# Kernel optimization log

Hardware: AMD Instinct MI355X
Metric: run time of the kernel (lower is better)

Reference implementation:

```python
import jax, jax.numpy as jnp
import numpy as np

NUM_HEADS = 16
KEY_DEPTH = 1024


def setup_inputs() -> dict:
    key = jax.random.key(0)
    ks = jax.random.split(key, 7)
    B, L, D = 2, 2048, 1024
    scale = 1.0 / np.sqrt(D)
    return {
        "query_antecedent": jax.random.normal(ks[0], (B, L, D), jnp.float32),
        "memory_antecedent": jax.random.normal(ks[1], (B, L, D), jnp.float32),
        "bias": jax.random.normal(ks[2], (1, 1, L, L), jnp.float32),
        "Wq": jax.random.normal(ks[3], (D, KEY_DEPTH), jnp.float32) * scale,
        "Wk": jax.random.normal(ks[4], (D, KEY_DEPTH), jnp.float32) * scale,
        "Wv": jax.random.normal(ks[5], (D, KEY_DEPTH), jnp.float32) * scale,
        "Wo": jax.random.normal(ks[6], (KEY_DEPTH, D), jnp.float32) * scale,
    }


def _split_heads(x, h):
    # [B, L, D] -> [B, H, L, D/H]
    b, l, d = x.shape
    return x.reshape(b, l, h, d // h).transpose(0, 2, 1, 3)


def reference(query_antecedent, memory_antecedent, bias, Wq, Wk, Wv, Wo):
    h = NUM_HEADS
    d_head = KEY_DEPTH // h
    q = _split_heads(query_antecedent @ Wq, h) * (d_head ** -0.5)
    k = _split_heads(memory_antecedent @ Wk, h)
    v = _split_heads(memory_antecedent @ Wv, h)
    # [B, H, Lq, Lk]
    logits = jnp.einsum("bhqd,bhkd->bhqk", q, k) + bias
    weights = jax.nn.softmax(logits, axis=-1)
    x = jnp.einsum("bhqk,bhkd->bhqd", weights, v)
    # combine heads: [B, H, L, d] -> [B, L, H*d]
    b, _, l, d = x.shape
    x = x.transpose(0, 2, 1, 3).reshape(b, l, h * d)
    return x @ Wo
```

## Files before the change

### kernel.cpp

```cpp
#include <hip/hip_runtime.h>
#include <hip/hip_bf16.h>


typedef __attribute__((ext_vector_type(8))) short short8;
typedef __attribute__((ext_vector_type(4))) short short4v;
typedef __attribute__((ext_vector_type(4))) float float4v;

#define BATCH 2
#define LSEQ 2048
#define DMODEL 1024
#define NHEADS 16
#define DHEAD 64
#define MROWS 4096
#define QKVLD 3072

__global__ __launch_bounds__(256)
void convert_kernel(const float* __restrict__ qa, const float* __restrict__ ma,
                    __hip_bfloat16* __restrict__ qo, __hip_bfloat16* __restrict__ mo)
{
    const size_t i = ((size_t)blockIdx.x * 256 + threadIdx.x) * 8;
    const float* src = blockIdx.y ? ma : qa;
    __hip_bfloat16* dst = blockIdx.y ? mo : qo;
    float4 v0 = *reinterpret_cast<const float4*>(src + i);
    float4 v1 = *reinterpret_cast<const float4*>(src + i + 4);
    union { __hip_bfloat16 h[8]; int4 v; } pk;
    pk.h[0] = (__hip_bfloat16)v0.x; pk.h[1] = (__hip_bfloat16)v0.y;
    pk.h[2] = (__hip_bfloat16)v0.z; pk.h[3] = (__hip_bfloat16)v0.w;
    pk.h[4] = (__hip_bfloat16)v1.x; pk.h[5] = (__hip_bfloat16)v1.y;
    pk.h[6] = (__hip_bfloat16)v1.z; pk.h[7] = (__hip_bfloat16)v1.w;
    *reinterpret_cast<int4*>(dst + i) = pk.v;
}

__global__ __launch_bounds__(256)
void transpose_w_kernel(const float* __restrict__ W0, const float* __restrict__ W1,
                        const float* __restrict__ W2, const float* __restrict__ W3,
                        __hip_bfloat16* __restrict__ T0, __hip_bfloat16* __restrict__ T1,
                        __hip_bfloat16* __restrict__ T2, __hip_bfloat16* __restrict__ T3)
{
    __shared__ __hip_bfloat16 T[64][68];

    const float* W; __hip_bfloat16* D;
    if      (blockIdx.z == 0) { W = W0; D = T0; }
    else if (blockIdx.z == 1) { W = W1; D = T1; }
    else if (blockIdx.z == 2) { W = W2; D = T2; }
    else                      { W = W3; D = T3; }

    const int t  = threadIdx.x;
    const int n0 = blockIdx.x * 64;
    const int k0 = blockIdx.y * 64;

#pragma unroll
    for (int p = 0; p < 4; ++p) {
        const int r = p * 16 + (t >> 4);
        const int c = (t & 15) * 4;
        float4 v = *reinterpret_cast<const float4*>(&W[(size_t)(k0 + r) * DMODEL + n0 + c]);
        union { __hip_bfloat16 h[4]; ushort4 v; } pk;
        pk.h[0] = (__hip_bfloat16)v.x; pk.h[1] = (__hip_bfloat16)v.y;
        pk.h[2] = (__hip_bfloat16)v.z; pk.h[3] = (__hip_bfloat16)v.w;
        *reinterpret_cast<ushort4*>(&T[r][c]) = pk.v;
    }
    __syncthreads();
#pragma unroll
    for (int p = 0; p < 2; ++p) {
        const int n  = p * 32 + (t & 31);
        const int kc = (t >> 5) * 8;
        union { __hip_bfloat16 h[8]; int4 v; } pk;
#pragma unroll
        for (int j = 0; j < 8; ++j) pk.h[j] = T[kc + j][n];
        *reinterpret_cast<int4*>(&D[(size_t)(n0 + n) * DMODEL + k0 + kc]) = pk.v;
    }
}

#define GBK 64

template<int BMT>
__global__ __launch_bounds__(256, 2)
void gemm_bt_kernel(const __hip_bfloat16* __restrict__ A0,
                    const __hip_bfloat16* __restrict__ A1, int nsplit,
                    float alpha0, float alpha1,
                    const __hip_bfloat16* __restrict__ Bt,
                    float* __restrict__ Cf, __hip_bfloat16* __restrict__ Cb,
                    int K, int ldc, int nbx)
{
    __shared__ __hip_bfloat16 As[BMT][GBK];
    __shared__ __hip_bfloat16 Bs[128][GBK];

    const int t    = threadIdx.x;
    const int w    = t >> 6;
    const int lane = t & 63;
    const int l15  = lane & 15;
    const int lq   = lane >> 4;
    const int wm   = (w >> 1) * (BMT / 2);
    const int wn   = (w & 1) * 64;
    const int MI   = BMT / 32;

    const int nwg  = gridDim.x;
    const int c    = blockIdx.x & 7;
    const int q    = blockIdx.x >> 3;
    const int mper = (nwg >> 3) / nbx;
    const int m0   = (c * mper + q / nbx) * BMT;
    const int n0   = (q % nbx) * 128;

    const __hip_bfloat16* A = (n0 < nsplit) ? A0 : A1;
    const float alpha = (n0 < nsplit) ? alpha0 : alpha1;

    const int lrow = lane >> 3;
    const int lch  = (lane & 7) ^ lrow;

    float4v acc[BMT / 32][4];
#pragma unroll
    for (int mi = 0; mi < MI; ++mi)
#pragma unroll
        for (int ni = 0; ni < 4; ++ni) acc[mi][ni] = (float4v){0.f, 0.f, 0.f, 0.f};

    for (int k0 = 0; k0 < K; k0 += GBK) {
        __syncthreads();
#pragma unroll
        for (int i = 0; i < BMT / 32; ++i) {
            const int rb = (w * (BMT / 32) + i) * 8;
            const int r  = rb + lrow;
            __builtin_amdgcn_global_load_lds(
                (const __attribute__((address_space(1))) void*)
                    (A + (size_t)(m0 + r) * K + k0 + lch * 8),
                (__attribute__((address_space(3))) void*)&As[rb][0], 16, 0, 0);
        }
#pragma unroll
        for (int i = 0; i < 4; ++i) {
            const int rb = (w * 4 + i) * 8;
            const int r  = rb + lrow;
            __builtin_amdgcn_global_load_lds(
                (const __attribute__((address_space(1))) void*)
                    (Bt + (size_t)(n0 + r) * K + k0 + lch * 8),
                (__attribute__((address_space(3))) void*)&Bs[rb][0], 16, 0, 0);
        }
        asm volatile("s_waitcnt vmcnt(0)" ::: "memory");
        __syncthreads();

#pragma unroll
        for (int kh = 0; kh < 2; ++kh) {
            short8 af[BMT / 32], bf[4];
#pragma unroll
            for (int mi = 0; mi < MI; ++mi) {
                const int r = wm + mi * 16 + l15;
                af[mi] = *reinterpret_cast<const short8*>(
                    &As[r][(((kh << 2) | lq) ^ (r & 7)) << 3]);
            }
#pragma unroll
            for (int ni = 0; ni < 4; ++ni) {
                const int r = wn + ni * 16 + l15;
                bf[ni] = *reinterpret_cast<const short8*>(
                    &Bs[r][(((kh << 2) | lq) ^ (r & 7)) << 3]);
            }
#pragma unroll
            for (int mi = 0; mi < MI; ++mi)
#pragma unroll
                for (int ni = 0; ni < 4; ++ni)
                    acc[mi][ni] = __builtin_amdgcn_mfma_f32_16x16x32_bf16(
                        af[mi], bf[ni], acc[mi][ni], 0, 0, 0);
        }
    }

#pragma unroll
    for (int mi = 0; mi < MI; ++mi)
#pragma unroll
        for (int ni = 0; ni < 4; ++ni)
#pragma unroll
            for (int r = 0; r < 4; ++r) {
                const int row = m0 + wm + mi * 16 + lq * 4 + r;
                const int col = n0 + wn + ni * 16 + l15;
                const float v = acc[mi][ni][r] * alpha;
                if (Cf) Cf[(size_t)row * ldc + col] = v;
                else    Cb[(size_t)row * ldc + col] = (__hip_bfloat16)v;
            }
}

#define KSTR 68
#define PSTR 132
#define NT (LSEQ / 128)

__global__ __launch_bounds__(512, 4)
void attn_mfma_kernel(const __hip_bfloat16* __restrict__ QKV,
                      const float* __restrict__ bias,
                      __hip_bfloat16* __restrict__ X)
{
    __shared__ __hip_bfloat16 Ks[2][128][KSTR];
    __shared__ __hip_bfloat16 Vt[2][64][PSTR];

    const int t   = threadIdx.x;
    const int w   = t >> 6;
    const int l15 = t & 15;
    const int lq  = (t & 63) >> 4;

    const int bid = blockIdx.x;
    const int r8  = bid & 7;
    const int j   = bid >> 3;
    const int bh  = r8 + 8 * (j >> 4);
    const int q0  = (j & 15) * 128;
    const int b   = bh >> 4;
    const int h   = bh & 15;

    const __hip_bfloat16* Kb = QKV + (size_t)b * LSEQ * QKVLD + 1024 + h * DHEAD;
    const __hip_bfloat16* Vb = Kb + 1024;

    short8 aq[2];
    {
        const __hip_bfloat16* qrow = QKV +
            (size_t)(b * LSEQ + q0 + w * 16 + l15) * QKVLD + h * DHEAD + lq * 8;
        aq[0] = *reinterpret_cast<const short8*>(qrow);
        aq[1] = *reinterpret_cast<const short8*>(qrow + 32);
    }

    const float* bp = bias + (size_t)(q0 + w * 16 + l15) * LSEQ + lq * 4;

    float lsum = 0.f;
    float4v o_acc[4];
#pragma unroll
    for (int n = 0; n < 4; ++n) o_acc[n] = (float4v){0.f, 0.f, 0.f, 0.f};

    const int skey = t >> 2;
    const int sdh  = (t & 3) * 16;
    const int a    = t & 3;
    const int cblk = ((skey >> 5) << 2) | ((skey >> 2) & 3);
    const int vcol = (((cblk ^ (a << 2)) << 3)) | ((((skey >> 4) & 1) << 2)) | (skey & 3);

    int4 pk0, pk1, pv0, pv1;
    {
        const __hip_bfloat16* ks = Kb + (size_t)skey * QKVLD + sdh;
        pk0 = *reinterpret_cast<const int4*>(ks);
        pk1 = *reinterpret_cast<const int4*>(ks + 8);
        const __hip_bfloat16* vs = Vb + (size_t)skey * QKVLD + sdh;
        pv0 = *reinterpret_cast<const int4*>(vs);
        pv1 = *reinterpret_cast<const int4*>(vs + 8);
    }
    *reinterpret_cast<int4*>(&Ks[0][skey][sdh])     = pk0;
    *reinterpret_cast<int4*>(&Ks[0][skey][sdh + 8]) = pk1;
    {
        const __hip_bfloat16* vp0 = reinterpret_cast<const __hip_bfloat16*>(&pv0);
        const __hip_bfloat16* vp1 = reinterpret_cast<const __hip_bfloat16*>(&pv1);
#pragma unroll
        for (int jj = 0; jj < 8; ++jj) Vt[0][sdh + jj][vcol]     = vp0[jj];
#pragma unroll
        for (int jj = 0; jj < 8; ++jj) Vt[0][sdh + 8 + jj][vcol] = vp1[jj];
    }
    {
        const __hip_bfloat16* ks = Kb + (size_t)(128 + skey) * QKVLD + sdh;
        pk0 = *reinterpret_cast<const int4*>(ks);
        pk1 = *reinterpret_cast<const int4*>(ks + 8);
        const __hip_bfloat16* vs = Vb + (size_t)(128 + skey) * QKVLD + sdh;
        pv0 = *reinterpret_cast<const int4*>(vs);
        pv1 = *reinterpret_cast<const int4*>(vs + 8);
    }
    __syncthreads();

    for (int kt = 0; kt < NT; ++kt) {
        const int cur = kt & 1;
        const int k0  = kt * 128;

        if (kt < NT - 1) {
            *reinterpret_cast<int4*>(&Ks[cur ^ 1][skey][sdh])     = pk0;
            *reinterpret_cast<int4*>(&Ks[cur ^ 1][skey][sdh + 8]) = pk1;
            const __hip_bfloat16* vp0 = reinterpret_cast<const __hip_bfloat16*>(&pv0);
            const __hip_bfloat16* vp1 = reinterpret_cast<const __hip_bfloat16*>(&pv1);
#pragma unroll
            for (int jj = 0; jj < 8; ++jj) Vt[cur ^ 1][sdh + jj][vcol]     = vp0[jj];
#pragma unroll
            for (int jj = 0; jj < 8; ++jj) Vt[cur ^ 1][sdh + 8 + jj][vcol] = vp1[jj];
            if (kt < NT - 2) {
                const int knext = k0 + 256;
                const __hip_bfloat16* ks = Kb + (size_t)(knext + skey) * QKVLD + sdh;
                pk0 = *reinterpret_cast<const int4*>(ks);
                pk1 = *reinterpret_cast<const int4*>(ks + 8);
                const __hip_bfloat16* vs = Vb + (size_t)(knext + skey) * QKVLD + sdh;
                pv0 = *reinterpret_cast<const int4*>(vs);
                pv1 = *reinterpret_cast<const int4*>(vs + 8);
            }
        }

#pragma unroll
        for (int m = 0; m < 4; ++m) {
            short8 bkA0 = *reinterpret_cast<const short8*>(&Ks[cur][(2*m)    *16 + l15][lq * 8]);
            short8 bkA1 = *reinterpret_cast<const short8*>(&Ks[cur][(2*m)    *16 + l15][32 + lq * 8]);
            short8 bkB0 = *reinterpret_cast<const short8*>(&Ks[cur][(2*m + 1)*16 + l15][lq * 8]);
            short8 bkB1 = *reinterpret_cast<const short8*>(&Ks[cur][(2*m + 1)*16 + l15][32 + lq * 8]);
            float4v bvA = *reinterpret_cast<const float4v*>(bp + k0 + 32 * m);
            float4v bvB = *reinterpret_cast<const float4v*>(bp + k0 + 32 * m + 16);

            float4v sA = (float4v){0.f, 0.f, 0.f, 0.f};
            float4v sB = (float4v){0.f, 0.f, 0.f, 0.f};
            __builtin_amdgcn_s_setprio(1);
            sA = __builtin_amdgcn_mfma_f32_16x16x32_bf16(bkA0, aq[0], sA, 0, 0, 0);
            sA = __builtin_amdgcn_mfma_f32_16x16x32_bf16(bkA1, aq[1], sA, 0, 0, 0);
            sB = __builtin_amdgcn_mfma_f32_16x16x32_bf16(bkB0, aq[0], sB, 0, 0, 0);
            sB = __builtin_amdgcn_mfma_f32_16x16x32_bf16(bkB1, aq[1], sB, 0, 0, 0);
            __builtin_amdgcn_s_setprio(0);

            union { __hip_bfloat16 hh[8]; short8 v; } pp;
#pragma unroll
            for (int e = 0; e < 4; ++e) {
                const float ev = __expf(sA[e] + bvA[e]);
                lsum += ev;
                pp.hh[e] = (__hip_bfloat16)ev;
            }
#pragma unroll
            for (int e = 0; e < 4; ++e) {
                const float ev = __expf(sB[e] + bvB[e]);
                lsum += ev;
                pp.hh[4 + e] = (__hip_bfloat16)ev;
            }
            const short8 pf = pp.v;

            short8 vt[4];
#pragma unroll
            for (int n = 0; n < 4; ++n)
                vt[n] = *reinterpret_cast<const short8*>(
                    &Vt[cur][n * 16 + l15][((m * 4 + lq) ^ (n << 2)) << 3]);

            __builtin_amdgcn_s_setprio(1);
#pragma unroll
            for (int n = 0; n < 4; ++n)
                o_acc[n] = __builtin_amdgcn_mfma_f32_16x16x32_bf16(
                    vt[n], pf, o_acc[n], 0, 0, 0);
            __builtin_amdgcn_s_setprio(0);
        }
        __syncthreads();
    }

    lsum += __shfl_xor(lsum, 16);
    lsum += __shfl_xor(lsum, 32);
    const float inv = 1.f / lsum;
    {
        const int row = q0 + w * 16 + l15;
        __hip_bfloat16* dst = X + (size_t)(b * LSEQ + row) * DMODEL + h * DHEAD + lq * 4;
#pragma unroll
        for (int n = 0; n < 4; ++n) {
            union { __hip_bfloat16 hh[4]; short4v v; } o;
#pragma unroll
            for (int e = 0; e < 4; ++e) o.hh[e] = (__hip_bfloat16)(o_acc[n][e] * inv);
            *reinterpret_cast<short4v*>(dst + n * 16) = o.v;
        }
    }
}

extern "C" void kernel_launch(void* const* d_in, const int* in_sizes, int n_in,
                              void* d_out, int out_size, void* d_ws, size_t ws_size,
                              hipStream_t stream)
{
    const float* qa   = (const float*)d_in[0];
    const float* ma   = (const float*)d_in[1];
    const float* bias = (const float*)d_in[2];
    const float* Wq   = (const float*)d_in[3];
    const float* Wk   = (const float*)d_in[4];
    const float* Wv   = (const float*)d_in[5];
    const float* Wo   = (const float*)d_in[6];
    float* out = (float*)d_out;

    char* wsb = (char*)d_ws;
    __hip_bfloat16* qa16 = (__hip_bfloat16*)(wsb);
    __hip_bfloat16* ma16 = (__hip_bfloat16*)(wsb + (8u << 20));
    __hip_bfloat16* Wt   = (__hip_bfloat16*)(wsb + (16u << 20));
    __hip_bfloat16* Wot  = (__hip_bfloat16*)(wsb + (22u << 20));
    __hip_bfloat16* QKVw = (__hip_bfloat16*)(wsb + (24u << 20));
    __hip_bfloat16* Xw   = qa16;

    convert_kernel<<<dim3(MROWS * DMODEL / (256 * 8), 2), 256, 0, stream>>>(
        qa, ma, qa16, ma16);

    transpose_w_kernel<<<dim3(16, 16, 4), 256, 0, stream>>>(
        Wq, Wk, Wv, Wo,
        Wt, Wt + (size_t)DMODEL * DMODEL, Wt + 2 * (size_t)DMODEL * DMODEL, Wot);

    gemm_bt_kernel<128><<<dim3(768), 256, 0, stream>>>(
        qa16, ma16, DMODEL, 0.125f, 1.0f, Wt, nullptr, QKVw, DMODEL, QKVLD, 24);

    attn_mfma_kernel<<<dim3(512), 512, 0, stream>>>(QKVw, bias, Xw);

    gemm_bt_kernel<64><<<dim3(512), 256, 0, stream>>>(
        Xw, Xw, DMODEL + 1, 1.0f, 1.0f, Wot, out, nullptr, DMODEL, DMODEL, 8);
}
```

Baseline: 235.2 us.

## Double-buffer GEMM LDS tiles and reorder weight-transpose store mapping

```diff
diff --git a/kernel.cpp b/kernel.cpp
--- a/kernel.cpp
+++ b/kernel.cpp
@@ -62,8 +62,8 @@
     __syncthreads();
 #pragma unroll
     for (int p = 0; p < 2; ++p) {
-        const int n  = p * 32 + (t & 31);
-        const int kc = (t >> 5) * 8;
+        const int n  = p * 32 + (t >> 3);
+        const int kc = (t & 7) * 8;
         union { __hip_bfloat16 h[8]; int4 v; } pk;
 #pragma unroll
         for (int j = 0; j < 8; ++j) pk.h[j] = T[kc + j][n];
@@ -82,8 +82,8 @@
                     float* __restrict__ Cf, __hip_bfloat16* __restrict__ Cb,
                     int K, int ldc, int nbx)
 {
-    __shared__ __hip_bfloat16 As[BMT][GBK];
-    __shared__ __hip_bfloat16 Bs[128][GBK];
+    __shared__ __hip_bfloat16 As[2][BMT][GBK];
+    __shared__ __hip_bfloat16 Bs[2][128][GBK];
 
     const int t    = threadIdx.x;
     const int w    = t >> 6;
@@ -113,16 +113,15 @@
 #pragma unroll
         for (int ni = 0; ni < 4; ++ni) acc[mi][ni] = (float4v){0.f, 0.f, 0.f, 0.f};
 
-    for (int k0 = 0; k0 < K; k0 += GBK) {
-        __syncthreads();
+    auto stage = [&](int bb, int kk) {
 #pragma unroll
         for (int i = 0; i < BMT / 32; ++i) {
             const int rb = (w * (BMT / 32) + i) * 8;
             const int r  = rb + lrow;
             __builtin_amdgcn_global_load_lds(
                 (const __attribute__((address_space(1))) void*)
-                    (A + (size_t)(m0 + r) * K + k0 + lch * 8),
-                (__attribute__((address_space(3))) void*)&As[rb][0], 16, 0, 0);
+                    (A + (size_t)(m0 + r) * K + kk + lch * 8),
+                (__attribute__((address_space(3))) void*)&As[bb][rb][0], 16, 0, 0);
         }
 #pragma unroll
         for (int i = 0; i < 4; ++i) {
@@ -130,10 +129,26 @@
             const int r  = rb + lrow;
             __builtin_amdgcn_global_load_lds(
                 (const __attribute__((address_space(1))) void*)
-                    (Bt + (size_t)(n0 + r) * K + k0 + lch * 8),
-                (__attribute__((address_space(3))) void*)&Bs[rb][0], 16, 0, 0);
-        }
-        asm volatile("s_waitcnt vmcnt(0)" ::: "memory");
+                    (Bt + (size_t)(n0 + r) * K + kk + lch * 8),
+                (__attribute__((address_space(3))) void*)&Bs[bb][rb][0], 16, 0, 0);
+        }
+    };
+
+    stage(0, 0);
+
+    int it = 0;
+    for (int k0 = 0; k0 < K; k0 += GBK, ++it) {
+        const int cur = it & 1;
+        __syncthreads();
+        if (k0 + GBK < K) {
+            stage(cur ^ 1, k0 + GBK);
+            if constexpr (BMT == 128)
+                asm volatile("s_waitcnt vmcnt(8)" ::: "memory");
+            else
+                asm volatile("s_waitcnt vmcnt(6)" ::: "memory");
+        } else {
+            asm volatile("s_waitcnt vmcnt(0)" ::: "memory");
+        }
         __syncthreads();
 
 #pragma unroll
@@ -143,13 +158,13 @@
             for (int mi = 0; mi < MI; ++mi) {
                 const int r = wm + mi * 16 + l15;
                 af[mi] = *reinterpret_cast<const short8*>(
-                    &As[r][(((kh << 2) | lq) ^ (r & 7)) << 3]);
+                    &As[cur][r][(((kh << 2) | lq) ^ (r & 7)) << 3]);
             }
 #pragma unroll
             for (int ni = 0; ni < 4; ++ni) {
                 const int r = wn + ni * 16 + l15;
                 bf[ni] = *reinterpret_cast<const short8*>(
-                    &Bs[r][(((kh << 2) | lq) ^ (r & 7)) << 3]);
+                    &Bs[cur][r][(((kh << 2) | lq) ^ (r & 7)) << 3]);
             }
 #pragma unroll
             for (int mi = 0; mi < MI; ++mi)
```

Result: slower. 243.6 us (+3.6%).

## Shrink attention blocks to 64 queries with single-buffered K/V tiles

Applied to the files above, without the earlier changes.

```diff
diff --git a/kernel.cpp b/kernel.cpp
--- a/kernel.cpp
+++ b/kernel.cpp
@@ -62,8 +62,8 @@
     __syncthreads();
 #pragma unroll
     for (int p = 0; p < 2; ++p) {
-        const int n  = p * 32 + (t & 31);
-        const int kc = (t >> 5) * 8;
+        const int n  = p * 32 + (t >> 3);
+        const int kc = (t & 7) * 8;
         union { __hip_bfloat16 h[8]; int4 v; } pk;
 #pragma unroll
         for (int j = 0; j < 8; ++j) pk.h[j] = T[kc + j][n];
@@ -176,15 +176,14 @@
 
 #define KSTR 68
 #define PSTR 132
-#define NT (LSEQ / 128)
-
-__global__ __launch_bounds__(512, 4)
+
+__global__ __launch_bounds__(256, 4)
 void attn_mfma_kernel(const __hip_bfloat16* __restrict__ QKV,
                       const float* __restrict__ bias,
                       __hip_bfloat16* __restrict__ X)
 {
-    __shared__ __hip_bfloat16 Ks[2][128][KSTR];
-    __shared__ __hip_bfloat16 Vt[2][64][PSTR];
+    __shared__ __hip_bfloat16 Ks[128][KSTR];
+    __shared__ __hip_bfloat16 Vt[64][PSTR];
 
     const int t   = threadIdx.x;
     const int w   = t >> 6;
@@ -194,8 +193,8 @@
     const int bid = blockIdx.x;
     const int r8  = bid & 7;
     const int j   = bid >> 3;
-    const int bh  = r8 + 8 * (j >> 4);
-    const int q0  = (j & 15) * 128;
+    const int bh  = r8 + 8 * (j >> 5);
+    const int q0  = (j & 31) * 64;
     const int b   = bh >> 4;
     const int h   = bh & 15;
 
@@ -217,71 +216,64 @@
 #pragma unroll
     for (int n = 0; n < 4; ++n) o_acc[n] = (float4v){0.f, 0.f, 0.f, 0.f};
 
-    const int skey = t >> 2;
-    const int sdh  = (t & 3) * 16;
-    const int a    = t & 3;
+    const int skey = t >> 1;
+    const int sdh  = (t & 1) * 32;
+    const int a0   = (t & 1) * 2;
     const int cblk = ((skey >> 5) << 2) | ((skey >> 2) & 3);
-    const int vcol = (((cblk ^ (a << 2)) << 3)) | ((((skey >> 4) & 1) << 2)) | (skey & 3);
-
-    int4 pk0, pk1, pv0, pv1;
+    const int vlo  = ((((skey >> 4) & 1) << 2)) | (skey & 3);
+    const int vcolA = ((cblk ^ (a0 << 2)) << 3) | vlo;
+    const int vcolB = ((cblk ^ ((a0 + 1) << 2)) << 3) | vlo;
+
+    int4 pk[4], pv[4];
     {
         const __hip_bfloat16* ks = Kb + (size_t)skey * QKVLD + sdh;
-        pk0 = *reinterpret_cast<const int4*>(ks);
-        pk1 = *reinterpret_cast<const int4*>(ks + 8);
         const __hip_bfloat16* vs = Vb + (size_t)skey * QKVLD + sdh;
-        pv0 = *reinterpret_cast<const int4*>(vs);
-        pv1 = *reinterpret_cast<const int4*>(vs + 8);
-    }
-    *reinterpret_cast<int4*>(&Ks[0][skey][sdh])     = pk0;
-    *reinterpret_cast<int4*>(&Ks[0][skey][sdh + 8]) = pk1;
-    {
-        const __hip_bfloat16* vp0 = reinterpret_cast<const __hip_bfloat16*>(&pv0);
-        const __hip_bfloat16* vp1 = reinterpret_cast<const __hip_bfloat16*>(&pv1);
-#pragma unroll
-        for (int jj = 0; jj < 8; ++jj) Vt[0][sdh + jj][vcol]     = vp0[jj];
-#pragma unroll
-        for (int jj = 0; jj < 8; ++jj) Vt[0][sdh + 8 + jj][vcol] = vp1[jj];
-    }
-    {
-        const __hip_bfloat16* ks = Kb + (size_t)(128 + skey) * QKVLD + sdh;
-        pk0 = *reinterpret_cast<const int4*>(ks);
-        pk1 = *reinterpret_cast<const int4*>(ks + 8);
-        const __hip_bfloat16* vs = Vb + (size_t)(128 + skey) * QKVLD + sdh;
-        pv0 = *reinterpret_cast<const int4*>(vs);
-        pv1 = *reinterpret_cast<const int4*>(vs + 8);
-    }
-    __syncthreads();
-
-    for (int kt = 0; kt < NT; ++kt) {
-        const int cur = kt & 1;
-        const int k0  = kt * 128;
-
-        if (kt < NT - 1) {
-            *reinterpret_cast<int4*>(&Ks[cur ^ 1][skey][sdh])     = pk0;
-            *reinterpret_cast<int4*>(&Ks[cur ^ 1][skey][sdh + 8]) = pk1;
-            const __hip_bfloat16* vp0 = reinterpret_cast<const __hip_bfloat16*>(&pv0);
-            const __hip_bfloat16* vp1 = reinterpret_cast<const __hip_bfloat16*>(&pv1);
-#pragma unroll
-            for (int jj = 0; jj < 8; ++jj) Vt[cur ^ 1][sdh + jj][vcol]     = vp0[jj];
-#pragma unroll
-            for (int jj = 0; jj < 8; ++jj) Vt[cur ^ 1][sdh + 8 + jj][vcol] = vp1[jj];
-            if (kt < NT - 2) {
-                const int knext = k0 + 256;
-                const __hip_bfloat16* ks = Kb + (size_t)(knext + skey) * QKVLD + sdh;
-                pk0 = *reinterpret_cast<const int4*>(ks);
-                pk1 = *reinterpret_cast<const int4*>(ks + 8);
-                const __hip_bfloat16* vs = Vb + (size_t)(knext + skey) * QKVLD + sdh;
-                pv0 = *reinterpret_cast<const int4*>(vs);
-                pv1 = *reinterpret_cast<const int4*>(vs + 8);
-            }
-        }
+#pragma unroll
+        for (int i = 0; i < 4; ++i) {
+            pk[i] = *reinterpret_cast<const int4*>(ks + 8 * i);
+            pv[i] = *reinterpret_cast<const int4*>(vs + 8 * i);
+        }
+    }
+
+    for (int kt = 0; kt < LSEQ / 128; ++kt) {
+        const int k0 = kt * 128;
+        __syncthreads();
+#pragma unroll
+        for (int i = 0; i < 4; ++i)
+            *reinterpret_cast<int4*>(&Ks[skey][sdh + 8 * i]) = pk[i];
+        {
+            const __hip_bfloat16* v0 = reinterpret_cast<const __hip_bfloat16*>(&pv[0]);
+            const __hip_bfloat16* v1 = reinterpret_cast<const __hip_bfloat16*>(&pv[1]);
+            const __hip_bfloat16* v2 = reinterpret_cast<const __hip_bfloat16*>(&pv[2]);
+            const __hip_bfloat16* v3 = reinterpret_cast<const __hip_bfloat16*>(&pv[3]);
+            const int d0 = a0 * 16;
+#pragma unroll
+            for (int jj = 0; jj < 8; ++jj) Vt[d0 + jj][vcolA]      = v0[jj];
+#pragma unroll
+            for (int jj = 0; jj < 8; ++jj) Vt[d0 + 8 + jj][vcolA]  = v1[jj];
+#pragma unroll
+            for (int jj = 0; jj < 8; ++jj) Vt[d0 + 16 + jj][vcolB] = v2[jj];
+#pragma unroll
+            for (int jj = 0; jj < 8; ++jj) Vt[d0 + 24 + jj][vcolB] = v3[jj];
+        }
+        {
+            const int knext = (kt + 1 < LSEQ / 128) ? k0 + 128 : k0;
+            const __hip_bfloat16* ks = Kb + (size_t)(knext + skey) * QKVLD + sdh;
+            const __hip_bfloat16* vs = Vb + (size_t)(knext + skey) * QKVLD + sdh;
+#pragma unroll
+            for (int i = 0; i < 4; ++i) {
+                pk[i] = *reinterpret_cast<const int4*>(ks + 8 * i);
+                pv[i] = *reinterpret_cast<const int4*>(vs + 8 * i);
+            }
+        }
+        __syncthreads();
 
 #pragma unroll
         for (int m = 0; m < 4; ++m) {
-            short8 bkA0 = *reinterpret_cast<const short8*>(&Ks[cur][(2*m)    *16 + l15][lq * 8]);
-            short8 bkA1 = *reinterpret_cast<const short8*>(&Ks[cur][(2*m)    *16 + l15][32 + lq * 8]);
-            short8 bkB0 = *reinterpret_cast<const short8*>(&Ks[cur][(2*m + 1)*16 + l15][lq * 8]);
-            short8 bkB1 = *reinterpret_cast<const short8*>(&Ks[cur][(2*m + 1)*16 + l15][32 + lq * 8]);
+            short8 bkA0 = *reinterpret_cast<const short8*>(&Ks[(2*m)    *16 + l15][lq * 8]);
+            short8 bkA1 = *reinterpret_cast<const short8*>(&Ks[(2*m)    *16 + l15][32 + lq * 8]);
+            short8 bkB0 = *reinterpret_cast<const short8*>(&Ks[(2*m + 1)*16 + l15][lq * 8]);
+            short8 bkB1 = *reinterpret_cast<const short8*>(&Ks[(2*m + 1)*16 + l15][32 + lq * 8]);
             float4v bvA = *reinterpret_cast<const float4v*>(bp + k0 + 32 * m);
             float4v bvB = *reinterpret_cast<const float4v*>(bp + k0 + 32 * m + 16);
 
@@ -313,7 +305,7 @@
 #pragma unroll
             for (int n = 0; n < 4; ++n)
                 vt[n] = *reinterpret_cast<const short8*>(
-                    &Vt[cur][n * 16 + l15][((m * 4 + lq) ^ (n << 2)) << 3]);
+                    &Vt[n * 16 + l15][((m * 4 + lq) ^ (n << 2)) << 3]);
 
             __builtin_amdgcn_s_setprio(1);
 #pragma unroll
@@ -322,7 +314,6 @@
                     vt[n], pf, o_acc[n], 0, 0, 0);
             __builtin_amdgcn_s_setprio(0);
         }
-        __syncthreads();
     }
 
     lsum += __shfl_xor(lsum, 16);
@@ -372,7 +363,7 @@
     gemm_bt_kernel<128><<<dim3(768), 256, 0, stream>>>(
         qa16, ma16, DMODEL, 0.125f, 1.0f, Wt, nullptr, QKVw, DMODEL, QKVLD, 24);
 
-    attn_mfma_kernel<<<dim3(512), 512, 0, stream>>>(QKVw, bias, Xw);
+    attn_mfma_kernel<<<dim3(1024), 256, 0, stream>>>(QKVw, bias, Xw);
 
     gemm_bt_kernel<64><<<dim3(512), 256, 0, stream>>>(
         Xw, Xw, DMODEL + 1, 1.0f, 1.0f, Wot, out, nullptr, DMODEL, DMODEL, 8);
```

After: 344.1 us. 46.3% more time.

## Load K fragments directly from global into registers, dropping K shared tile

Applied to the files above, without the earlier changes.

```diff
diff --git a/kernel.cpp b/kernel.cpp
--- a/kernel.cpp
+++ b/kernel.cpp
@@ -62,8 +62,8 @@
     __syncthreads();
 #pragma unroll
     for (int p = 0; p < 2; ++p) {
-        const int n  = p * 32 + (t & 31);
-        const int kc = (t >> 5) * 8;
+        const int n  = p * 32 + (t >> 3);
+        const int kc = (t & 7) * 8;
         union { __hip_bfloat16 h[8]; int4 v; } pk;
 #pragma unroll
         for (int j = 0; j < 8; ++j) pk.h[j] = T[kc + j][n];
@@ -174,7 +174,6 @@
             }
 }
 
-#define KSTR 68
 #define PSTR 132
 #define NT (LSEQ / 128)
 
@@ -183,7 +182,6 @@
                       const float* __restrict__ bias,
                       __hip_bfloat16* __restrict__ X)
 {
-    __shared__ __hip_bfloat16 Ks[2][128][KSTR];
     __shared__ __hip_bfloat16 Vt[2][64][PSTR];
 
     const int t   = threadIdx.x;
@@ -223,17 +221,14 @@
     const int cblk = ((skey >> 5) << 2) | ((skey >> 2) & 3);
     const int vcol = (((cblk ^ (a << 2)) << 3)) | ((((skey >> 4) & 1) << 2)) | (skey & 3);
 
-    int4 pk0, pk1, pv0, pv1;
-    {
-        const __hip_bfloat16* ks = Kb + (size_t)skey * QKVLD + sdh;
-        pk0 = *reinterpret_cast<const int4*>(ks);
-        pk1 = *reinterpret_cast<const int4*>(ks + 8);
+    const __hip_bfloat16* kfp = Kb + (size_t)l15 * QKVLD + lq * 8;
+
+    int4 pv0, pv1;
+    {
         const __hip_bfloat16* vs = Vb + (size_t)skey * QKVLD + sdh;
         pv0 = *reinterpret_cast<const int4*>(vs);
         pv1 = *reinterpret_cast<const int4*>(vs + 8);
     }
-    *reinterpret_cast<int4*>(&Ks[0][skey][sdh])     = pk0;
-    *reinterpret_cast<int4*>(&Ks[0][skey][sdh + 8]) = pk1;
     {
         const __hip_bfloat16* vp0 = reinterpret_cast<const __hip_bfloat16*>(&pv0);
         const __hip_bfloat16* vp1 = reinterpret_cast<const __hip_bfloat16*>(&pv1);
@@ -243,13 +238,20 @@
         for (int jj = 0; jj < 8; ++jj) Vt[0][sdh + 8 + jj][vcol] = vp1[jj];
     }
     {
-        const __hip_bfloat16* ks = Kb + (size_t)(128 + skey) * QKVLD + sdh;
-        pk0 = *reinterpret_cast<const int4*>(ks);
-        pk1 = *reinterpret_cast<const int4*>(ks + 8);
         const __hip_bfloat16* vs = Vb + (size_t)(128 + skey) * QKVLD + sdh;
         pv0 = *reinterpret_cast<const int4*>(vs);
         pv1 = *reinterpret_cast<const int4*>(vs + 8);
     }
+
+    short8 kf[2][4];
+    {
+        const __hip_bfloat16* p0 = kfp;
+        const __hip_bfloat16* p1 = kfp + 16 * QKVLD;
+        kf[0][0] = *reinterpret_cast<const short8*>(p0);
+        kf[0][1] = *reinterpret_cast<const short8*>(p0 + 32);
+        kf[0][2] = *reinterpret_cast<const short8*>(p1);
+        kf[0][3] = *reinterpret_cast<const short8*>(p1 + 32);
+    }
     __syncthreads();
 
     for (int kt = 0; kt < NT; ++kt) {
@@ -257,8 +259,6 @@
         const int k0  = kt * 128;
 
         if (kt < NT - 1) {
-            *reinterpret_cast<int4*>(&Ks[cur ^ 1][skey][sdh])     = pk0;
-            *reinterpret_cast<int4*>(&Ks[cur ^ 1][skey][sdh + 8]) = pk1;
             const __hip_bfloat16* vp0 = reinterpret_cast<const __hip_bfloat16*>(&pv0);
             const __hip_bfloat16* vp1 = reinterpret_cast<const __hip_bfloat16*>(&pv1);
 #pragma unroll
@@ -266,11 +266,7 @@
 #pragma unroll
             for (int jj = 0; jj < 8; ++jj) Vt[cur ^ 1][sdh + 8 + jj][vcol] = vp1[jj];
             if (kt < NT - 2) {
-                const int knext = k0 + 256;
-                const __hip_bfloat16* ks = Kb + (size_t)(knext + skey) * QKVLD + sdh;
-                pk0 = *reinterpret_cast<const int4*>(ks);
-                pk1 = *reinterpret_cast<const int4*>(ks + 8);
-                const __hip_bfloat16* vs = Vb + (size_t)(knext + skey) * QKVLD + sdh;
+                const __hip_bfloat16* vs = Vb + (size_t)(k0 + 256 + skey) * QKVLD + sdh;
                 pv0 = *reinterpret_cast<const int4*>(vs);
                 pv1 = *reinterpret_cast<const int4*>(vs + 8);
             }
@@ -278,21 +274,28 @@
 
 #pragma unroll
         for (int m = 0; m < 4; ++m) {
-            short8 bkA0 = *reinterpret_cast<const short8*>(&Ks[cur][(2*m)    *16 + l15][lq * 8]);
-            short8 bkA1 = *reinterpret_cast<const short8*>(&Ks[cur][(2*m)    *16 + l15][32 + lq * 8]);
-            short8 bkB0 = *reinterpret_cast<const short8*>(&Ks[cur][(2*m + 1)*16 + l15][lq * 8]);
-            short8 bkB1 = *reinterpret_cast<const short8*>(&Ks[cur][(2*m + 1)*16 + l15][32 + lq * 8]);
             float4v bvA = *reinterpret_cast<const float4v*>(bp + k0 + 32 * m);
             float4v bvB = *reinterpret_cast<const float4v*>(bp + k0 + 32 * m + 16);
 
             float4v sA = (float4v){0.f, 0.f, 0.f, 0.f};
             float4v sB = (float4v){0.f, 0.f, 0.f, 0.f};
             __builtin_amdgcn_s_setprio(1);
-            sA = __builtin_amdgcn_mfma_f32_16x16x32_bf16(bkA0, aq[0], sA, 0, 0, 0);
-            sA = __builtin_amdgcn_mfma_f32_16x16x32_bf16(bkA1, aq[1], sA, 0, 0, 0);
-            sB = __builtin_amdgcn_mfma_f32_16x16x32_bf16(bkB0, aq[0], sB, 0, 0, 0);
-            sB = __builtin_amdgcn_mfma_f32_16x16x32_bf16(bkB1, aq[1], sB, 0, 0, 0);
+            sA = __builtin_amdgcn_mfma_f32_16x16x32_bf16(kf[m & 1][0], aq[0], sA, 0, 0, 0);
+            sA = __builtin_amdgcn_mfma_f32_16x16x32_bf16(kf[m & 1][1], aq[1], sA, 0, 0, 0);
+            sB = __builtin_amdgcn_mfma_f32_16x16x32_bf16(kf[m & 1][2], aq[0], sB, 0, 0, 0);
+            sB = __builtin_amdgcn_mfma_f32_16x16x32_bf16(kf[m & 1][3], aq[1], sB, 0, 0, 0);
             __builtin_amdgcn_s_setprio(0);
+
+            {
+                const int knext = (m < 3) ? (k0 + (2 * m + 2) * 16)
+                                          : ((kt + 1 < NT) ? (kt + 1) * 128 : k0);
+                const __hip_bfloat16* p0 = kfp + (size_t)knext * QKVLD;
+                const __hip_bfloat16* p1 = p0 + 16 * QKVLD;
+                kf[(m + 1) & 1][0] = *reinterpret_cast<const short8*>(p0);
+                kf[(m + 1) & 1][1] = *reinterpret_cast<const short8*>(p0 + 32);
+                kf[(m + 1) & 1][2] = *reinterpret_cast<const short8*>(p1);
+                kf[(m + 1) & 1][3] = *reinterpret_cast<const short8*>(p1 + 32);
+            }
 
             union { __hip_bfloat16 hh[8]; short8 v; } pp;
 #pragma unroll
```

Measured after the change: 331.9 us. +41.1%, slower.
